# Kernel tuning notes

Measured on AMD Instinct MI355X. Metric: run time of the kernel, lower is better.

Reference implementation:

```python
import jax, jax.numpy as jnp
import numpy as np

NUM_ATOMS = 100
D = 32        # initial_atom_dim
H = 16        # hidden_dim (multiplicity per irrep)
NB = 16       # edge_dim / number of bessel basis functions
CUT = 6.0     # radius_cutoff
DEG = 4.0     # degree_norm
OUT = 1       # output_dim
INV4PI = 1.0 / np.sqrt(4.0 * np.pi)  # 'integral' SH normalization


def _bessel(d, nb, cut):
    # e3nn soft_one_hot_linspace(basis='bessel', cutoff=True) * sqrt(nb)
    x = d[:, None]
    n = jnp.arange(1, nb + 1, dtype=d.dtype)
    safe = jnp.maximum(x, 1e-9)
    out = np.sqrt(2.0 / cut) * jnp.sin(n * jnp.pi * x / cut) / safe
    return out * (x < cut) * np.sqrt(float(nb))


def _fc(x, w1, w2):
    # e3nn FullyConnectedNet: fan-in normalized linear layers, silu, no bias
    h = jax.nn.silu(x @ w1 / np.sqrt(x.shape[-1]))
    return h @ w2 / np.sqrt(w1.shape[-1])


def _forward(atomic_numbers, edge_index, coords, atom_emb,
             fc0_w1, fc0_w2, fc1_w1, fc1_w2, w_readout):
    src, dst = edge_index[0], edge_index[1]
    N = coords.shape[0]
    E = src.shape[0]

    vec = coords[src] - coords[dst]                      # [E,3]
    dist = jnp.linalg.norm(vec, axis=-1)                 # [E]
    unit = vec / jnp.maximum(dist, 1e-9)[:, None]

    # spherical harmonics, l=0 and l=1, 'integral' normalization
    y0 = jnp.full((E,), INV4PI, dtype=coords.dtype)      # [E]
    y1 = (np.sqrt(3.0) * INV4PI) * unit                  # [E,3]
    basis = _bessel(dist, NB, CUT)                       # [E,NB]

    x = atom_emb[atomic_numbers]                         # [N,D] (row 0 is padding)

    # ---- layer 0: scalars (D x0e) x (1x0e+1x1o) -> H x0e + H x1o ----
    w = _fc(basis, fc0_w1, fc0_w2)                       # [E, 2*D*H] per-edge TP weights
    wa = w[:, : D * H].reshape(E, D, H)
    wb = w[:, D * H:].reshape(E, D, H)
    xs = x[src]
    n0 = 1.0 / np.sqrt(D)                                # path fan-in norm
    m0 = jnp.einsum('ed,edh->eh', xs, wa) * y0[:, None] * n0          # [E,H]
    m1 = jnp.einsum('ed,edh->eh', xs, wb)[:, :, None] * y1[:, None, :] * n0  # [E,H,3]
    z0 = jax.ops.segment_sum(m0, dst, num_segments=N) / DEG           # [N,H]
    z1 = jax.ops.segment_sum(m1, dst, num_segments=N) / DEG           # [N,H,3]

    # ---- layer 1: (H x0e + H x1o) x (1x0e+1x1o) -> same irreps, skip-connected ----
    w = _fc(basis, fc1_w1, fc1_w2)                       # [E, 4*H*H]
    w1_ = w[:, 0 * H * H:1 * H * H].reshape(E, H, H)     # 0e x 0e -> 0e
    w2_ = w[:, 1 * H * H:2 * H * H].reshape(E, H, H)     # 0e x 1o -> 1o
    w3_ = w[:, 2 * H * H:3 * H * H].reshape(E, H, H)     # 1o x 0e -> 1o
    w4_ = w[:, 3 * H * H:4 * H * H].reshape(E, H, H)     # 1o x 1o -> 0e (CG = dot/sqrt(3))
    s, v = z0[src], z1[src]
    n1 = 1.0 / np.sqrt(2 * H)                            # two paths per output irrep
    dot = jnp.einsum('ehm,em->eh', v, y1) / np.sqrt(3.0)
    o0 = (jnp.einsum('eh,ehk->ek', s, w1_) * y0[:, None]
          + jnp.einsum('eh,ehk->ek', dot, w4_)) * n1
    o1 = (jnp.einsum('eh,ehk->ek', s, w2_)[:, :, None] * y1[:, None, :]
          + jnp.einsum('ehm,ehk->ekm', v, w3_) * y0[:, None, None]) * n1
    z0 = jax.ops.segment_sum(o0, dst, num_segments=N) / DEG + z0      # skip
    z1 = jax.ops.segment_sum(o1, dst, num_segments=N) / DEG + z1

    # ---- scalar readout (o3.Linear onto 0e) + graph sum-pool ----
    node_scalar = z0 @ w_readout / np.sqrt(H)            # [N,OUT]
    return jnp.sum(node_scalar, axis=0)                  # [OUT]


def setup_inputs() -> dict:
    key = jax.random.key(0)
    ks = jax.random.split(key, 9)
    N, E = 10000, 160000
    atomic_numbers = jax.random.randint(ks[0], (N,), 0, NUM_ATOMS)
    coords = jax.random.normal(ks[1], (N, 3), dtype=jnp.float32)
    edge_index = jax.random.randint(ks[2], (2, E), 0, N)
    atom_emb = jax.random.normal(ks[3], (NUM_ATOMS, D), dtype=jnp.float32).at[0].set(0.0)
    fc0_w1 = jax.random.normal(ks[4], (NB, H), dtype=jnp.float32)
    fc0_w2 = jax.random.normal(ks[5], (H, 2 * D * H), dtype=jnp.float32)
    fc1_w1 = jax.random.normal(ks[6], (NB, H), dtype=jnp.float32)
    fc1_w2 = jax.random.normal(ks[7], (H, 4 * H * H), dtype=jnp.float32)
    w_readout = jax.random.normal(ks[8], (H, OUT), dtype=jnp.float32)
    return {"atomic_numbers": atomic_numbers, "coords": coords, "edge_index": edge_index,
            "atom_emb": atom_emb, "fc0_w1": fc0_w1, "fc0_w2": fc0_w2,
            "fc1_w1": fc1_w1, "fc1_w2": fc1_w2, "w_readout": w_readout}


def reference(atomic_numbers, coords, edge_index, atom_emb,
              fc0_w1, fc0_w2, fc1_w1, fc1_w2, w_readout):
    return _forward(atomic_numbers, edge_index, coords, atom_emb,
                    fc0_w1, fc0_w2, fc1_w1, fc1_w2, w_readout)
```

## Files before the change

### kernel.cpp

```cpp
#include <hip/hip_runtime.h>
#include <math.h>


namespace {
constexpr int   NATOMS   = 100;
constexpr int   CAP      = 64;
constexpr float PI_F     = 3.14159265358979323846f;
constexpr float INV4PI_F = 0.28209479177387814f;
constexpr float SQRT3_F  = 1.7320508075688772f;
constexpr float CUT_F    = 6.0f;
constexpr float BASIS_C  = 2.3094010767585034f;
constexpr float N0_F     = 0.17677669529663687f;
constexpr float K0_F = INV4PI_F * N0_F * 0.0625f;
constexpr float K1_F = SQRT3_F * INV4PI_F * N0_F * 0.0625f;
}

__device__ __forceinline__ float silu_fast(float x) {
  return x / (1.0f + __expf(-x));
}

__device__ __forceinline__ float block_reduce_sum(float v) {
  #pragma unroll
  for (int o = 32; o > 0; o >>= 1) v += __shfl_down(v, o, 64);
  __shared__ float ls[8];
  int lane = threadIdx.x & 63;
  int w    = threadIdx.x >> 6;
  if (lane == 0) ls[w] = v;
  __syncthreads();
  float s = 0.f;
  if (threadIdx.x == 0) {
    int nw = (blockDim.x + 63) >> 6;
    for (int i = 0; i < nw; ++i) s += ls[i];
  }
  return s;
}

__global__ void precompute_kernel(const float* __restrict__ atom_emb,
                                  const float* __restrict__ fc0_w2,
                                  const float* __restrict__ fc1_w2,
                                  const float* __restrict__ w_readout,
                                  float* __restrict__ T0, float* __restrict__ T1,
                                  float* __restrict__ G1, float* __restrict__ G4) {
  int b = blockIdx.x;
  int t = threadIdx.x;
  int j = t >> 4;
  int h = t & 15;
  if (b < NATOMS) {
    float s0 = 0.f, s1 = 0.f;
    #pragma unroll
    for (int d = 0; d < 32; ++d) {
      float x = atom_emb[b * 32 + d];
      s0 = fmaf(x, fc0_w2[j * 1024 + d * 16 + h], s0);
      s1 = fmaf(x, fc0_w2[j * 1024 + 512 + d * 16 + h], s1);
    }
    T0[b * 256 + t] = s0;
    T1[b * 256 + t] = s1;
  } else {
    float g1 = 0.f, g4 = 0.f;
    #pragma unroll
    for (int k = 0; k < 16; ++k) {
      float r = w_readout[k];
      g1 = fmaf(fc1_w2[j * 1024 + h * 16 + k], r, g1);
      g4 = fmaf(fc1_w2[j * 1024 + 768 + h * 16 + k], r, g4);
    }
    G1[t] = g1;
    G4[t] = g4;
  }
}

__global__ void bucket_kernel(const int* __restrict__ ei,
                              int* __restrict__ cursor,
                              int* __restrict__ elist, int E) {
  int e = blockIdx.x * blockDim.x + threadIdx.x;
  if (e < E) {
    int d = ei[E + e];
    int pos = atomicAdd(&cursor[d], 1);
    if (pos < CAP) elist[d * CAP + pos] = ei[e];
  }
}

__global__ void __launch_bounds__(256, 4)
gather_kernel(const int* __restrict__ elist,
              const int* __restrict__ cursor,
              const float* __restrict__ coords,
              const int* __restrict__ an,
              const float* __restrict__ fc0_w1,
              const float* __restrict__ T0,
              const float* __restrict__ T1,
              const float* __restrict__ G1t,
              const float* __restrict__ G4t,
              const float* __restrict__ w_readout,
              float* __restrict__ zbuf,
              float* __restrict__ out,
              int N) {
  __shared__ float ggs[512];
  ggs[threadIdx.x]       = G1t[threadIdx.x];
  ggs[256 + threadIdx.x] = G4t[threadIdx.x];
  __syncthreads();

  int wave = threadIdx.x >> 6;
  int lane = threadIdx.x & 63;
  int g    = lane >> 4;
  int t    = lane & 15;
  int base = lane & 48;
  int node = blockIdx.x * 4 + wave;
  bool valid = node < N;

  float w0c[16];
  #pragma unroll
  for (int k = 0; k < 16; ++k) w0c[k] = fc0_w1[k * 16 + t];
  float rr = w_readout[t];

  float cnx = 0.f, cny = 0.f, cnz = 0.f;
  int cnt = 0;
  if (valid) {
    cnx = coords[3 * node + 0];
    cny = coords[3 * node + 1];
    cnz = coords[3 * node + 2];
    cnt = min(cursor[node], CAP);
  }

  const float angc = PI_F / CUT_F;
  float acc0 = 0.f, accx = 0.f, accy = 0.f, accz = 0.f;
  for (int i = g; i < cnt; i += 4) {
    int s = elist[node * CAP + i];
    float vx = coords[3 * s + 0] - cnx;
    float vy = coords[3 * s + 1] - cny;
    float vz = coords[3 * s + 2] - cnz;
    float dist = sqrtf(vx * vx + vy * vy + vz * vz);
    float inv  = 1.0f / fmaxf(dist, 1e-9f);
    float ux = vx * inv, uy = vy * inv, uz = vz * inv;
    float bc = (dist < CUT_F) ? (BASIS_C * inv) : 0.0f;

    float ang = angc * dist;
    float sc = __sinf(ang);
    float tw = 2.0f * __cosf(ang);
    float sp = 0.f, acc = 0.f;
    #pragma unroll
    for (int k = 0; k < 16; ++k) {
      acc = fmaf(sc, w0c[k], acc);
      float sn = fmaf(tw, sc, -sp);
      sp = sc; sc = sn;
    }
    float h0t = silu_fast(acc * bc * 0.25f);

    int a = an[s];
    const float* t0 = T0 + a * 256 + t;
    const float* t1 = T1 + a * 256 + t;
    float u0 = 0.f, u1 = 0.f;
    #pragma unroll
    for (int j = 0; j < 16; ++j) {
      float hj = __shfl(h0t, base + j, 64);
      u0 = fmaf(hj, t0[j * 16], u0);
      u1 = fmaf(hj, t1[j * 16], u1);
    }
    acc0 += u0;
    accx = fmaf(u1, ux, accx);
    accy = fmaf(u1, uy, accy);
    accz = fmaf(u1, uz, accz);
  }
  acc0 += __shfl_xor(acc0, 16, 64); acc0 += __shfl_xor(acc0, 32, 64);
  accx += __shfl_xor(accx, 16, 64); accx += __shfl_xor(accx, 32, 64);
  accy += __shfl_xor(accy, 16, 64); accy += __shfl_xor(accy, 32, 64);
  accz += __shfl_xor(accz, 16, 64); accz += __shfl_xor(accz, 32, 64);

  float srcv = (g == 0) ? acc0 * K0_F
                        : ((g == 1) ? accx : (g == 2) ? accy : accz) * K1_F;
  int tofs = (g == 0) ? 0 : 256;
  float o = 0.f;
  #pragma unroll
  for (int h = 0; h < 16; ++h) {
    float vh = __shfl(srcv, base + h, 64);
    o = fmaf(ggs[tofs + t * 16 + h], vh, o);
  }
  if (valid) zbuf[(size_t)node * 64 + lane] = o;

  float p = (valid && g == 0) ? acc0 * K0_F * rr : 0.f;
  float tot = block_reduce_sum(p);
  if (threadIdx.x == 0) atomicAdd(out, tot * 0.25f);
}

__global__ void __launch_bounds__(256, 4)
phase2_kernel(const int* __restrict__ ei,
              const float* __restrict__ coords,
              const float* __restrict__ fc1_w1,
              const float* __restrict__ zbuf,
              float* __restrict__ out,
              int E) {
  int t = threadIdx.x & 15;
  float w1c[16];
  #pragma unroll
  for (int k = 0; k < 16; ++k) w1c[k] = fc1_w1[k * 16 + t];

  int gid = (blockIdx.x * blockDim.x + threadIdx.x) >> 4;
  int ngroups = (gridDim.x * blockDim.x) >> 4;
  const float angc = PI_F / CUT_F;

  float c = 0.f;
  for (int e = gid; e < E; e += ngroups) {
    int s = ei[e];
    int d = ei[E + e];
    float vx = coords[3 * s + 0] - coords[3 * d + 0];
    float vy = coords[3 * s + 1] - coords[3 * d + 1];
    float vz = coords[3 * s + 2] - coords[3 * d + 2];
    float dist = sqrtf(vx * vx + vy * vy + vz * vz);
    float inv  = 1.0f / fmaxf(dist, 1e-9f);
    float ux = vx * inv, uy = vy * inv, uz = vz * inv;
    float bc = (dist < CUT_F) ? (BASIS_C * inv) : 0.0f;

    float ang = angc * dist;
    float sc = __sinf(ang);
    float tw = 2.0f * __cosf(ang);
    float sp = 0.f, acc = 0.f;
    #pragma unroll
    for (int k = 0; k < 16; ++k) {
      acc = fmaf(sc, w1c[k], acc);
      float sn = fmaf(tw, sc, -sp);
      sp = sc; sc = sn;
    }
    float h1t = silu_fast(acc * bc * 0.25f);

    const float* zb = zbuf + (size_t)s * 64;
    float q  = zb[t];
    float px = zb[16 + t];
    float py = zb[32 + t];
    float pz = zb[48 + t];
    c = fmaf(h1t, fmaf(px, ux, fmaf(py, uy, fmaf(pz, uz, q))), c);
  }
  c *= INV4PI_F * N0_F * (1.0f / 64.0f);
  float tot = block_reduce_sum(c);
  if (threadIdx.x == 0) atomicAdd(out, tot);
}

extern "C" void kernel_launch(void* const* d_in, const int* in_sizes, int n_in,
                              void* d_out, int out_size, void* d_ws, size_t ws_size,
                              hipStream_t stream) {
  const int*   an        = (const int*)d_in[0];
  const float* coords    = (const float*)d_in[1];
  const int*   ei        = (const int*)d_in[2];
  const float* atom_emb  = (const float*)d_in[3];
  const float* fc0_w1    = (const float*)d_in[4];
  const float* fc0_w2    = (const float*)d_in[5];
  const float* fc1_w1    = (const float*)d_in[6];
  const float* fc1_w2    = (const float*)d_in[7];
  const float* w_readout = (const float*)d_in[8];

  int N = in_sizes[0];
  int E = in_sizes[2] / 2;

  float* ws   = (float*)d_ws;
  float* zbuf = ws;
  float* T0   = zbuf + (size_t)N * 64;
  float* T1   = T0 + NATOMS * 256;
  float* G1   = T1 + NATOMS * 256;
  float* G4   = G1 + 256;
  int*   cursor = (int*)(G4 + 256);
  int*   elist  = cursor + N;
  float* out = (float*)d_out;

  hipMemsetAsync(cursor, 0, (size_t)N * sizeof(int), stream);
  hipMemsetAsync(out, 0, sizeof(float), stream);

  precompute_kernel<<<NATOMS + 1, 256, 0, stream>>>(
      atom_emb, fc0_w2, fc1_w2, w_readout, T0, T1, G1, G4);

  int blk = 256;
  bucket_kernel<<<(E + blk - 1) / blk, blk, 0, stream>>>(ei, cursor, elist, E);

  gather_kernel<<<(N + 3) / 4, blk, 0, stream>>>(
      elist, cursor, coords, an, fc0_w1, T0, T1, G1, G4, w_readout,
      zbuf, out, N);

  phase2_kernel<<<2048, blk, 0, stream>>>(ei, coords, fc1_w1, zbuf, out, E);
}
```

Before: 165.8 us.

## Transpose T/G/zbuf layouts for vector loads, prefetch neighbors, shrink gather blocks

The precomputed T0/T1 and G1/G4 tables are stored transposed so that each lane reads its 16 weights as four float4 loads instead of strided scalars. zbuf is interleaved per hidden channel so phase2 fetches q,px,py,pz with a single float4 load. The gather loop software-prefetches the next neighbor's coordinates and atom type. Gather blocks shrink to 128 threads and phase2 uses half as many blocks. In exchange the loop holds more live registers, and the smaller blocks do more shared-memory setup and atomics per node.

```diff
diff --git a/kernel.cpp b/kernel.cpp
--- a/kernel.cpp
+++ b/kernel.cpp
@@ -39,12 +39,13 @@
                                   const float* __restrict__ fc0_w2,
                                   const float* __restrict__ fc1_w2,
                                   const float* __restrict__ w_readout,
-                                  float* __restrict__ T0, float* __restrict__ T1,
-                                  float* __restrict__ G1, float* __restrict__ G4) {
+                                  float* __restrict__ T0T, float* __restrict__ T1T,
+                                  float* __restrict__ G1T, float* __restrict__ G4T) {
   int b = blockIdx.x;
   int t = threadIdx.x;
   int j = t >> 4;
   int h = t & 15;
+  int tidx = h * 16 + j;
   if (b < NATOMS) {
     float s0 = 0.f, s1 = 0.f;
     #pragma unroll
@@ -53,8 +54,8 @@
       s0 = fmaf(x, fc0_w2[j * 1024 + d * 16 + h], s0);
       s1 = fmaf(x, fc0_w2[j * 1024 + 512 + d * 16 + h], s1);
     }
-    T0[b * 256 + t] = s0;
-    T1[b * 256 + t] = s1;
+    T0T[b * 256 + tidx] = s0;
+    T1T[b * 256 + tidx] = s1;
   } else {
     float g1 = 0.f, g4 = 0.f;
     #pragma unroll
@@ -63,8 +64,8 @@
       g1 = fmaf(fc1_w2[j * 1024 + h * 16 + k], r, g1);
       g4 = fmaf(fc1_w2[j * 1024 + 768 + h * 16 + k], r, g4);
     }
-    G1[t] = g1;
-    G4[t] = g4;
+    G1T[h * 16 + j] = g1;
+    G4T[h * 16 + j] = g4;
   }
 }
 
@@ -79,23 +80,28 @@
   }
 }
 
-__global__ void __launch_bounds__(256, 4)
+__global__ void __launch_bounds__(128)
 gather_kernel(const int* __restrict__ elist,
               const int* __restrict__ cursor,
               const float* __restrict__ coords,
               const int* __restrict__ an,
               const float* __restrict__ fc0_w1,
-              const float* __restrict__ T0,
-              const float* __restrict__ T1,
-              const float* __restrict__ G1t,
-              const float* __restrict__ G4t,
+              const float* __restrict__ T0T,
+              const float* __restrict__ T1T,
+              const float* __restrict__ G1T,
+              const float* __restrict__ G4T,
               const float* __restrict__ w_readout,
               float* __restrict__ zbuf,
               float* __restrict__ out,
               int N) {
   __shared__ float ggs[512];
-  ggs[threadIdx.x]       = G1t[threadIdx.x];
-  ggs[256 + threadIdx.x] = G4t[threadIdx.x];
+  {
+    int tt = threadIdx.x;
+    ggs[tt]       = G1T[tt];
+    ggs[tt + 128] = G1T[tt + 128];
+    ggs[tt + 256] = G4T[tt];
+    ggs[tt + 384] = G4T[tt + 128];
+  }
   __syncthreads();
 
   int wave = threadIdx.x >> 6;
@@ -103,7 +109,7 @@
   int g    = lane >> 4;
   int t    = lane & 15;
   int base = lane & 48;
-  int node = blockIdx.x * 4 + wave;
+  int node = blockIdx.x * 2 + wave;
   bool valid = node < N;
 
   float w0c[16];
@@ -122,11 +128,24 @@
 
   const float angc = PI_F / CUT_F;
   float acc0 = 0.f, accx = 0.f, accy = 0.f, accz = 0.f;
+
+  int s = (g < cnt) ? elist[node * CAP + g] : 0;
+  float sx = coords[3 * s + 0];
+  float sy = coords[3 * s + 1];
+  float sz = coords[3 * s + 2];
+  int   a  = an[s];
+
   for (int i = g; i < cnt; i += 4) {
-    int s = elist[node * CAP + i];
-    float vx = coords[3 * s + 0] - cnx;
-    float vy = coords[3 * s + 1] - cny;
-    float vz = coords[3 * s + 2] - cnz;
+    int inext = i + 4;
+    int sn = (inext < cnt) ? elist[node * CAP + inext] : 0;
+    float nsx = coords[3 * sn + 0];
+    float nsy = coords[3 * sn + 1];
+    float nsz = coords[3 * sn + 2];
+    int   na  = an[sn];
+
+    float vx = sx - cnx;
+    float vy = sy - cny;
+    float vz = sz - cnz;
     float dist = sqrtf(vx * vx + vy * vy + vz * vz);
     float inv  = 1.0f / fmaxf(dist, 1e-9f);
     float ux = vx * inv, uy = vy * inv, uz = vz * inv;
@@ -139,25 +158,33 @@
     #pragma unroll
     for (int k = 0; k < 16; ++k) {
       acc = fmaf(sc, w0c[k], acc);
-      float sn = fmaf(tw, sc, -sp);
-      sp = sc; sc = sn;
+      float sn2 = fmaf(tw, sc, -sp);
+      sp = sc; sc = sn2;
     }
     float h0t = silu_fast(acc * bc * 0.25f);
 
-    int a = an[s];
-    const float* t0 = T0 + a * 256 + t;
-    const float* t1 = T1 + a * 256 + t;
+    const float4* t0 = (const float4*)(T0T + a * 256 + t * 16);
+    const float4* t1 = (const float4*)(T1T + a * 256 + t * 16);
+    float4 A0 = t0[0], A1 = t0[1], A2 = t0[2], A3 = t0[3];
+    float4 B0 = t1[0], B1 = t1[1], B2 = t1[2], B3 = t1[3];
+    float r0[16] = {A0.x,A0.y,A0.z,A0.w, A1.x,A1.y,A1.z,A1.w,
+                    A2.x,A2.y,A2.z,A2.w, A3.x,A3.y,A3.z,A3.w};
+    float r1[16] = {B0.x,B0.y,B0.z,B0.w, B1.x,B1.y,B1.z,B1.w,
+                    B2.x,B2.y,B2.z,B2.w, B3.x,B3.y,B3.z,B3.w};
+
     float u0 = 0.f, u1 = 0.f;
     #pragma unroll
     for (int j = 0; j < 16; ++j) {
       float hj = __shfl(h0t, base + j, 64);
-      u0 = fmaf(hj, t0[j * 16], u0);
-      u1 = fmaf(hj, t1[j * 16], u1);
+      u0 = fmaf(hj, r0[j], u0);
+      u1 = fmaf(hj, r1[j], u1);
     }
     acc0 += u0;
     accx = fmaf(u1, ux, accx);
     accy = fmaf(u1, uy, accy);
     accz = fmaf(u1, uz, accz);
+
+    s = sn; sx = nsx; sy = nsy; sz = nsz; a = na;
   }
   acc0 += __shfl_xor(acc0, 16, 64); acc0 += __shfl_xor(acc0, 32, 64);
   accx += __shfl_xor(accx, 16, 64); accx += __shfl_xor(accx, 32, 64);
@@ -171,9 +198,9 @@
   #pragma unroll
   for (int h = 0; h < 16; ++h) {
     float vh = __shfl(srcv, base + h, 64);
-    o = fmaf(ggs[tofs + t * 16 + h], vh, o);
-  }
-  if (valid) zbuf[(size_t)node * 64 + lane] = o;
+    o = fmaf(ggs[tofs + h * 16 + t], vh, o);
+  }
+  if (valid) zbuf[(size_t)node * 64 + t * 4 + g] = o;
 
   float p = (valid && g == 0) ? acc0 * K0_F * rr : 0.f;
   float tot = block_reduce_sum(p);
@@ -220,12 +247,8 @@
     }
     float h1t = silu_fast(acc * bc * 0.25f);
 
-    const float* zb = zbuf + (size_t)s * 64;
-    float q  = zb[t];
-    float px = zb[16 + t];
-    float py = zb[32 + t];
-    float pz = zb[48 + t];
-    c = fmaf(h1t, fmaf(px, ux, fmaf(py, uy, fmaf(pz, uz, q))), c);
+    float4 z = ((const float4*)(zbuf + (size_t)s * 64))[t];
+    c = fmaf(h1t, fmaf(z.y, ux, fmaf(z.z, uy, fmaf(z.w, uz, z.x))), c);
   }
   c *= INV4PI_F * N0_F * (1.0f / 64.0f);
   float tot = block_reduce_sum(c);
@@ -250,11 +273,11 @@
 
   float* ws   = (float*)d_ws;
   float* zbuf = ws;
-  float* T0   = zbuf + (size_t)N * 64;
-  float* T1   = T0 + NATOMS * 256;
-  float* G1   = T1 + NATOMS * 256;
-  float* G4   = G1 + 256;
-  int*   cursor = (int*)(G4 + 256);
+  float* T0T  = zbuf + (size_t)N * 64;
+  float* T1T  = T0T + NATOMS * 256;
+  float* G1T  = T1T + NATOMS * 256;
+  float* G4T  = G1T + 256;
+  int*   cursor = (int*)(G4T + 256);
   int*   elist  = cursor + N;
   float* out = (float*)d_out;
 
@@ -262,14 +285,14 @@
   hipMemsetAsync(out, 0, sizeof(float), stream);
 
   precompute_kernel<<<NATOMS + 1, 256, 0, stream>>>(
-      atom_emb, fc0_w2, fc1_w2, w_readout, T0, T1, G1, G4);
+      atom_emb, fc0_w2, fc1_w2, w_readout, T0T, T1T, G1T, G4T);
 
   int blk = 256;
   bucket_kernel<<<(E + blk - 1) / blk, blk, 0, stream>>>(ei, cursor, elist, E);
 
-  gather_kernel<<<(N + 3) / 4, blk, 0, stream>>>(
-      elist, cursor, coords, an, fc0_w1, T0, T1, G1, G4, w_readout,
+  gather_kernel<<<(N + 1) / 2, 128, 0, stream>>>(
+      elist, cursor, coords, an, fc0_w1, T0T, T1T, G1T, G4T, w_readout,
       zbuf, out, N);
 
-  phase2_kernel<<<2048, blk, 0, stream>>>(ei, coords, fc1_w1, zbuf, out, E);
-}
+  phase2_kernel<<<1024, blk, 0, stream>>>(ei, coords, fc1_w1, zbuf, out, E);
+}
```

New measurement: 191.0 us. 1.15x slower.

## Merge setup kernels, process two edges per gather iteration, interleave zbuf for float4 reads

Applied to the files above, without the earlier changes.

Merges the weight-precompute and edge-bucketing kernels into one launch, which removes a launch and its serialization point. The gather loop now handles two edges per iteration so more independent loads and math are in flight. The zbuf layout becomes channel-interleaved, so phase2 reads each source's (q,px,py,pz) with a single float4 load instead of four strided scalar loads. The G matrices are stored transposed to match the new indexing. The costs are higher register pressure in the gather kernel and some wasted work on the padded second edge.

```diff
diff --git a/kernel.cpp b/kernel.cpp
--- a/kernel.cpp
+++ b/kernel.cpp
@@ -35,17 +35,20 @@
   return s;
 }
 
-__global__ void precompute_kernel(const float* __restrict__ atom_emb,
-                                  const float* __restrict__ fc0_w2,
-                                  const float* __restrict__ fc1_w2,
-                                  const float* __restrict__ w_readout,
-                                  float* __restrict__ T0, float* __restrict__ T1,
-                                  float* __restrict__ G1, float* __restrict__ G4) {
+__global__ void setup_kernel(const float* __restrict__ atom_emb,
+                             const float* __restrict__ fc0_w2,
+                             const float* __restrict__ fc1_w2,
+                             const float* __restrict__ w_readout,
+                             const int* __restrict__ ei,
+                             float* __restrict__ T0, float* __restrict__ T1,
+                             float* __restrict__ G1T, float* __restrict__ G4T,
+                             int* __restrict__ cursor, int* __restrict__ elist,
+                             int E) {
   int b = blockIdx.x;
-  int t = threadIdx.x;
-  int j = t >> 4;
-  int h = t & 15;
+  int tt = threadIdx.x;
   if (b < NATOMS) {
+    int j = tt >> 4;
+    int h = tt & 15;
     float s0 = 0.f, s1 = 0.f;
     #pragma unroll
     for (int d = 0; d < 32; ++d) {
@@ -53,9 +56,11 @@
       s0 = fmaf(x, fc0_w2[j * 1024 + d * 16 + h], s0);
       s1 = fmaf(x, fc0_w2[j * 1024 + 512 + d * 16 + h], s1);
     }
-    T0[b * 256 + t] = s0;
-    T1[b * 256 + t] = s1;
-  } else {
+    T0[b * 256 + tt] = s0;
+    T1[b * 256 + tt] = s1;
+  } else if (b == NATOMS) {
+    int j = tt >> 4;
+    int h = tt & 15;
     float g1 = 0.f, g4 = 0.f;
     #pragma unroll
     for (int k = 0; k < 16; ++k) {
@@ -63,19 +68,15 @@
       g1 = fmaf(fc1_w2[j * 1024 + h * 16 + k], r, g1);
       g4 = fmaf(fc1_w2[j * 1024 + 768 + h * 16 + k], r, g4);
     }
-    G1[t] = g1;
-    G4[t] = g4;
-  }
-}
-
-__global__ void bucket_kernel(const int* __restrict__ ei,
-                              int* __restrict__ cursor,
-                              int* __restrict__ elist, int E) {
-  int e = blockIdx.x * blockDim.x + threadIdx.x;
-  if (e < E) {
-    int d = ei[E + e];
-    int pos = atomicAdd(&cursor[d], 1);
-    if (pos < CAP) elist[d * CAP + pos] = ei[e];
+    G1T[h * 16 + j] = g1;
+    G4T[h * 16 + j] = g4;
+  } else {
+    int e = (b - NATOMS - 1) * blockDim.x + tt;
+    if (e < E) {
+      int d = ei[E + e];
+      int pos = atomicAdd(&cursor[d], 1);
+      if (pos < CAP) elist[d * CAP + pos] = ei[e];
+    }
   }
 }
 
@@ -87,15 +88,15 @@
               const float* __restrict__ fc0_w1,
               const float* __restrict__ T0,
               const float* __restrict__ T1,
-              const float* __restrict__ G1t,
-              const float* __restrict__ G4t,
+              const float* __restrict__ G1T,
+              const float* __restrict__ G4T,
               const float* __restrict__ w_readout,
               float* __restrict__ zbuf,
               float* __restrict__ out,
               int N) {
   __shared__ float ggs[512];
-  ggs[threadIdx.x]       = G1t[threadIdx.x];
-  ggs[256 + threadIdx.x] = G4t[threadIdx.x];
+  ggs[threadIdx.x]       = G1T[threadIdx.x];
+  ggs[256 + threadIdx.x] = G4T[threadIdx.x];
   __syncthreads();
 
   int wave = threadIdx.x >> 6;
@@ -119,46 +120,66 @@
     cnz = coords[3 * node + 2];
     cnt = min(cursor[node], CAP);
   }
+  const int* eb = elist + (size_t)(valid ? node : 0) * CAP;
 
   const float angc = PI_F / CUT_F;
   float acc0 = 0.f, accx = 0.f, accy = 0.f, accz = 0.f;
-  for (int i = g; i < cnt; i += 4) {
-    int s = elist[node * CAP + i];
-    float vx = coords[3 * s + 0] - cnx;
-    float vy = coords[3 * s + 1] - cny;
-    float vz = coords[3 * s + 2] - cnz;
-    float dist = sqrtf(vx * vx + vy * vy + vz * vz);
-    float inv  = 1.0f / fmaxf(dist, 1e-9f);
-    float ux = vx * inv, uy = vy * inv, uz = vz * inv;
-    float bc = (dist < CUT_F) ? (BASIS_C * inv) : 0.0f;
-
-    float ang = angc * dist;
-    float sc = __sinf(ang);
-    float tw = 2.0f * __cosf(ang);
-    float sp = 0.f, acc = 0.f;
+
+  for (int i = g; i < cnt; i += 8) {
+    int iB = i + 4;
+    bool hasB = iB < cnt;
+    int sA = eb[i];
+    int sB = hasB ? eb[iB] : sA;
+
+    float pxA = coords[3 * sA + 0], pyA = coords[3 * sA + 1], pzA = coords[3 * sA + 2];
+    float pxB = coords[3 * sB + 0], pyB = coords[3 * sB + 1], pzB = coords[3 * sB + 2];
+    int aA = an[sA], aB = an[sB];
+
+    float vxA = pxA - cnx, vyA = pyA - cny, vzA = pzA - cnz;
+    float vxB = pxB - cnx, vyB = pyB - cny, vzB = pzB - cnz;
+    float dA = sqrtf(vxA * vxA + vyA * vyA + vzA * vzA);
+    float dB = sqrtf(vxB * vxB + vyB * vyB + vzB * vzB);
+    float ivA = 1.0f / fmaxf(dA, 1e-9f);
+    float ivB = 1.0f / fmaxf(dB, 1e-9f);
+    float uxA = vxA * ivA, uyA = vyA * ivA, uzA = vzA * ivA;
+    float uxB = vxB * ivB, uyB = vyB * ivB, uzB = vzB * ivB;
+    float bcA = (dA < CUT_F) ? (BASIS_C * ivA) : 0.0f;
+    float bcB = (dB < CUT_F) ? (BASIS_C * ivB) : 0.0f;
+
+    float angA = angc * dA, angB = angc * dB;
+    float scA = __sinf(angA), twA = 2.0f * __cosf(angA), spA = 0.f, hA = 0.f;
+    float scB = __sinf(angB), twB = 2.0f * __cosf(angB), spB = 0.f, hB = 0.f;
     #pragma unroll
     for (int k = 0; k < 16; ++k) {
-      acc = fmaf(sc, w0c[k], acc);
-      float sn = fmaf(tw, sc, -sp);
-      sp = sc; sc = sn;
-    }
-    float h0t = silu_fast(acc * bc * 0.25f);
-
-    int a = an[s];
-    const float* t0 = T0 + a * 256 + t;
-    const float* t1 = T1 + a * 256 + t;
-    float u0 = 0.f, u1 = 0.f;
+      hA = fmaf(scA, w0c[k], hA);
+      hB = fmaf(scB, w0c[k], hB);
+      float snA = fmaf(twA, scA, -spA); spA = scA; scA = snA;
+      float snB = fmaf(twB, scB, -spB); spB = scB; scB = snB;
+    }
+    float h0A = silu_fast(hA * bcA * 0.25f);
+    float h0B = silu_fast(hB * bcB * 0.25f);
+
+    const float* t0A = T0 + aA * 256 + t;
+    const float* t1A = T1 + aA * 256 + t;
+    const float* t0B = T0 + aB * 256 + t;
+    const float* t1B = T1 + aB * 256 + t;
+    float u0A = 0.f, u1A = 0.f, u0B = 0.f, u1B = 0.f;
     #pragma unroll
     for (int j = 0; j < 16; ++j) {
-      float hj = __shfl(h0t, base + j, 64);
-      u0 = fmaf(hj, t0[j * 16], u0);
-      u1 = fmaf(hj, t1[j * 16], u1);
-    }
-    acc0 += u0;
-    accx = fmaf(u1, ux, accx);
-    accy = fmaf(u1, uy, accy);
-    accz = fmaf(u1, uz, accz);
-  }
+      float hjA = __shfl(h0A, base + j, 64);
+      float hjB = __shfl(h0B, base + j, 64);
+      u0A = fmaf(hjA, t0A[j * 16], u0A);
+      u1A = fmaf(hjA, t1A[j * 16], u1A);
+      u0B = fmaf(hjB, t0B[j * 16], u0B);
+      u1B = fmaf(hjB, t1B[j * 16], u1B);
+    }
+    float mB = hasB ? 1.0f : 0.0f;
+    acc0 += u0A + mB * u0B;
+    accx = fmaf(u1A, uxA, fmaf(mB * u1B, uxB, accx));
+    accy = fmaf(u1A, uyA, fmaf(mB * u1B, uyB, accy));
+    accz = fmaf(u1A, uzA, fmaf(mB * u1B, uzB, accz));
+  }
+
   acc0 += __shfl_xor(acc0, 16, 64); acc0 += __shfl_xor(acc0, 32, 64);
   accx += __shfl_xor(accx, 16, 64); accx += __shfl_xor(accx, 32, 64);
   accy += __shfl_xor(accy, 16, 64); accy += __shfl_xor(accy, 32, 64);
@@ -171,9 +192,9 @@
   #pragma unroll
   for (int h = 0; h < 16; ++h) {
     float vh = __shfl(srcv, base + h, 64);
-    o = fmaf(ggs[tofs + t * 16 + h], vh, o);
-  }
-  if (valid) zbuf[(size_t)node * 64 + lane] = o;
+    o = fmaf(ggs[tofs + h * 16 + t], vh, o);
+  }
+  if (valid) zbuf[(size_t)node * 64 + t * 4 + g] = o;
 
   float p = (valid && g == 0) ? acc0 * K0_F * rr : 0.f;
   float tot = block_reduce_sum(p);
@@ -220,12 +241,8 @@
     }
     float h1t = silu_fast(acc * bc * 0.25f);
 
-    const float* zb = zbuf + (size_t)s * 64;
-    float q  = zb[t];
-    float px = zb[16 + t];
-    float py = zb[32 + t];
-    float pz = zb[48 + t];
-    c = fmaf(h1t, fmaf(px, ux, fmaf(py, uy, fmaf(pz, uz, q))), c);
+    float4 z = ((const float4*)(zbuf + (size_t)s * 64))[t];
+    c = fmaf(h1t, fmaf(z.y, ux, fmaf(z.z, uy, fmaf(z.w, uz, z.x))), c);
   }
   c *= INV4PI_F * N0_F * (1.0f / 64.0f);
   float tot = block_reduce_sum(c);
@@ -252,23 +269,23 @@
   float* zbuf = ws;
   float* T0   = zbuf + (size_t)N * 64;
   float* T1   = T0 + NATOMS * 256;
-  float* G1   = T1 + NATOMS * 256;
-  float* G4   = G1 + 256;
-  int*   cursor = (int*)(G4 + 256);
+  float* G1T  = T1 + NATOMS * 256;
+  float* G4T  = G1T + 256;
+  int*   cursor = (int*)(G4T + 256);
   int*   elist  = cursor + N;
   float* out = (float*)d_out;
 
   hipMemsetAsync(cursor, 0, (size_t)N * sizeof(int), stream);
   hipMemsetAsync(out, 0, sizeof(float), stream);
 
-  precompute_kernel<<<NATOMS + 1, 256, 0, stream>>>(
-      atom_emb, fc0_w2, fc1_w2, w_readout, T0, T1, G1, G4);
-
   int blk = 256;
-  bucket_kernel<<<(E + blk - 1) / blk, blk, 0, stream>>>(ei, cursor, elist, E);
+  int ebkts = (E + blk - 1) / blk;
+  setup_kernel<<<NATOMS + 1 + ebkts, blk, 0, stream>>>(
+      atom_emb, fc0_w2, fc1_w2, w_readout, ei,
+      T0, T1, G1T, G4T, cursor, elist, E);
 
   gather_kernel<<<(N + 3) / 4, blk, 0, stream>>>(
-      elist, cursor, coords, an, fc0_w1, T0, T1, G1, G4, w_readout,
+      elist, cursor, coords, an, fc0_w1, T0, T1, G1T, G4T, w_readout,
       zbuf, out, N);
 
   phase2_kernel<<<2048, blk, 0, stream>>>(ei, coords, fc1_w1, zbuf, out, E);
```

Result: no change. 165.0 us (-0.5%).

## Fuse precompute and bucketing, cache per-edge geometry, interleave zbuf layout

Applied to the files above, without the earlier changes.

Merges the weight precompute and edge bucketing into one setup kernel. That kernel also computes each edge's unit vector and distance once, storing them both in edge order and in the per-destination bucket along with the source atom type. The gather and phase2 kernels then read these records instead of recomputing geometry from coords, which removes scattered coordinate and atom-number gathers and one kernel launch. zbuf is stored interleaved so phase2 loads one float4 per lane. The cost is extra workspace traffic to write and read the edge records.

```diff
diff --git a/kernel.cpp b/kernel.cpp
--- a/kernel.cpp
+++ b/kernel.cpp
@@ -35,17 +35,25 @@
   return s;
 }
 
-__global__ void precompute_kernel(const float* __restrict__ atom_emb,
-                                  const float* __restrict__ fc0_w2,
-                                  const float* __restrict__ fc1_w2,
-                                  const float* __restrict__ w_readout,
-                                  float* __restrict__ T0, float* __restrict__ T1,
-                                  float* __restrict__ G1, float* __restrict__ G4) {
+__global__ void setup_kernel(const float* __restrict__ atom_emb,
+                             const float* __restrict__ fc0_w2,
+                             const float* __restrict__ fc1_w2,
+                             const float* __restrict__ w_readout,
+                             const int* __restrict__ ei,
+                             const float* __restrict__ coords,
+                             const int* __restrict__ an,
+                             float* __restrict__ T0, float* __restrict__ T1,
+                             float* __restrict__ G1T, float* __restrict__ G4T,
+                             int* __restrict__ cursor,
+                             float4* __restrict__ evec,
+                             float4* __restrict__ ebuf,
+                             int* __restrict__ ea,
+                             int E) {
   int b = blockIdx.x;
-  int t = threadIdx.x;
-  int j = t >> 4;
-  int h = t & 15;
+  int tt = threadIdx.x;
   if (b < NATOMS) {
+    int j = tt >> 4;
+    int h = tt & 15;
     float s0 = 0.f, s1 = 0.f;
     #pragma unroll
     for (int d = 0; d < 32; ++d) {
@@ -53,9 +61,11 @@
       s0 = fmaf(x, fc0_w2[j * 1024 + d * 16 + h], s0);
       s1 = fmaf(x, fc0_w2[j * 1024 + 512 + d * 16 + h], s1);
     }
-    T0[b * 256 + t] = s0;
-    T1[b * 256 + t] = s1;
-  } else {
+    T0[b * 256 + tt] = s0;
+    T1[b * 256 + tt] = s1;
+  } else if (b == NATOMS) {
+    int j = tt >> 4;
+    int h = tt & 15;
     float g1 = 0.f, g4 = 0.f;
     #pragma unroll
     for (int k = 0; k < 16; ++k) {
@@ -63,39 +73,45 @@
       g1 = fmaf(fc1_w2[j * 1024 + h * 16 + k], r, g1);
       g4 = fmaf(fc1_w2[j * 1024 + 768 + h * 16 + k], r, g4);
     }
-    G1[t] = g1;
-    G4[t] = g4;
-  }
-}
-
-__global__ void bucket_kernel(const int* __restrict__ ei,
-                              int* __restrict__ cursor,
-                              int* __restrict__ elist, int E) {
-  int e = blockIdx.x * blockDim.x + threadIdx.x;
-  if (e < E) {
-    int d = ei[E + e];
-    int pos = atomicAdd(&cursor[d], 1);
-    if (pos < CAP) elist[d * CAP + pos] = ei[e];
+    G1T[h * 16 + j] = g1;
+    G4T[h * 16 + j] = g4;
+  } else {
+    int e = (b - NATOMS - 1) * blockDim.x + tt;
+    if (e < E) {
+      int s = ei[e];
+      int d = ei[E + e];
+      float vx = coords[3 * s + 0] - coords[3 * d + 0];
+      float vy = coords[3 * s + 1] - coords[3 * d + 1];
+      float vz = coords[3 * s + 2] - coords[3 * d + 2];
+      float dist = sqrtf(vx * vx + vy * vy + vz * vz);
+      float inv  = 1.0f / fmaxf(dist, 1e-9f);
+      float4 rec = make_float4(vx * inv, vy * inv, vz * inv, dist);
+      evec[e] = rec;
+      int pos = atomicAdd(&cursor[d], 1);
+      if (pos < CAP) {
+        ebuf[d * CAP + pos] = rec;
+        ea[d * CAP + pos]   = an[s];
+      }
+    }
   }
 }
 
 __global__ void __launch_bounds__(256, 4)
-gather_kernel(const int* __restrict__ elist,
+gather_kernel(const float4* __restrict__ ebuf,
+              const int* __restrict__ ea,
               const int* __restrict__ cursor,
-              const float* __restrict__ coords,
-              const int* __restrict__ an,
               const float* __restrict__ fc0_w1,
               const float* __restrict__ T0,
               const float* __restrict__ T1,
-              const float* __restrict__ G1t,
-              const float* __restrict__ G4t,
+              const float* __restrict__ G1T,
+              const float* __restrict__ G4T,
               const float* __restrict__ w_readout,
               float* __restrict__ zbuf,
               float* __restrict__ out,
               int N) {
   __shared__ float ggs[512];
-  ggs[threadIdx.x]       = G1t[threadIdx.x];
-  ggs[256 + threadIdx.x] = G4t[threadIdx.x];
+  ggs[threadIdx.x]       = G1T[threadIdx.x];
+  ggs[256 + threadIdx.x] = G4T[threadIdx.x];
   __syncthreads();
 
   int wave = threadIdx.x >> 6;
@@ -111,26 +127,17 @@
   for (int k = 0; k < 16; ++k) w0c[k] = fc0_w1[k * 16 + t];
   float rr = w_readout[t];
 
-  float cnx = 0.f, cny = 0.f, cnz = 0.f;
-  int cnt = 0;
-  if (valid) {
-    cnx = coords[3 * node + 0];
-    cny = coords[3 * node + 1];
-    cnz = coords[3 * node + 2];
-    cnt = min(cursor[node], CAP);
-  }
+  int cnt = valid ? min(cursor[node], CAP) : 0;
+  int nb  = (valid ? node : 0) * CAP;
 
   const float angc = PI_F / CUT_F;
   float acc0 = 0.f, accx = 0.f, accy = 0.f, accz = 0.f;
+
   for (int i = g; i < cnt; i += 4) {
-    int s = elist[node * CAP + i];
-    float vx = coords[3 * s + 0] - cnx;
-    float vy = coords[3 * s + 1] - cny;
-    float vz = coords[3 * s + 2] - cnz;
-    float dist = sqrtf(vx * vx + vy * vy + vz * vz);
-    float inv  = 1.0f / fmaxf(dist, 1e-9f);
-    float ux = vx * inv, uy = vy * inv, uz = vz * inv;
-    float bc = (dist < CUT_F) ? (BASIS_C * inv) : 0.0f;
+    float4 ev = ebuf[nb + i];
+    int    a  = ea[nb + i];
+    float dist = ev.w;
+    float bc = (dist < CUT_F) ? (BASIS_C / fmaxf(dist, 1e-9f)) : 0.0f;
 
     float ang = angc * dist;
     float sc = __sinf(ang);
@@ -144,7 +151,6 @@
     }
     float h0t = silu_fast(acc * bc * 0.25f);
 
-    int a = an[s];
     const float* t0 = T0 + a * 256 + t;
     const float* t1 = T1 + a * 256 + t;
     float u0 = 0.f, u1 = 0.f;
@@ -155,10 +161,11 @@
       u1 = fmaf(hj, t1[j * 16], u1);
     }
     acc0 += u0;
-    accx = fmaf(u1, ux, accx);
-    accy = fmaf(u1, uy, accy);
-    accz = fmaf(u1, uz, accz);
-  }
+    accx = fmaf(u1, ev.x, accx);
+    accy = fmaf(u1, ev.y, accy);
+    accz = fmaf(u1, ev.z, accz);
+  }
+
   acc0 += __shfl_xor(acc0, 16, 64); acc0 += __shfl_xor(acc0, 32, 64);
   accx += __shfl_xor(accx, 16, 64); accx += __shfl_xor(accx, 32, 64);
   accy += __shfl_xor(accy, 16, 64); accy += __shfl_xor(accy, 32, 64);
@@ -171,9 +178,9 @@
   #pragma unroll
   for (int h = 0; h < 16; ++h) {
     float vh = __shfl(srcv, base + h, 64);
-    o = fmaf(ggs[tofs + t * 16 + h], vh, o);
-  }
-  if (valid) zbuf[(size_t)node * 64 + lane] = o;
+    o = fmaf(ggs[tofs + h * 16 + t], vh, o);
+  }
+  if (valid) zbuf[(size_t)node * 64 + t * 4 + g] = o;
 
   float p = (valid && g == 0) ? acc0 * K0_F * rr : 0.f;
   float tot = block_reduce_sum(p);
@@ -182,7 +189,7 @@
 
 __global__ void __launch_bounds__(256, 4)
 phase2_kernel(const int* __restrict__ ei,
-              const float* __restrict__ coords,
+              const float4* __restrict__ evec,
               const float* __restrict__ fc1_w1,
               const float* __restrict__ zbuf,
               float* __restrict__ out,
@@ -199,14 +206,9 @@
   float c = 0.f;
   for (int e = gid; e < E; e += ngroups) {
     int s = ei[e];
-    int d = ei[E + e];
-    float vx = coords[3 * s + 0] - coords[3 * d + 0];
-    float vy = coords[3 * s + 1] - coords[3 * d + 1];
-    float vz = coords[3 * s + 2] - coords[3 * d + 2];
-    float dist = sqrtf(vx * vx + vy * vy + vz * vz);
-    float inv  = 1.0f / fmaxf(dist, 1e-9f);
-    float ux = vx * inv, uy = vy * inv, uz = vz * inv;
-    float bc = (dist < CUT_F) ? (BASIS_C * inv) : 0.0f;
+    float4 ev = evec[e];
+    float dist = ev.w;
+    float bc = (dist < CUT_F) ? (BASIS_C / fmaxf(dist, 1e-9f)) : 0.0f;
 
     float ang = angc * dist;
     float sc = __sinf(ang);
@@ -220,12 +222,8 @@
     }
     float h1t = silu_fast(acc * bc * 0.25f);
 
-    const float* zb = zbuf + (size_t)s * 64;
-    float q  = zb[t];
-    float px = zb[16 + t];
-    float py = zb[32 + t];
-    float pz = zb[48 + t];
-    c = fmaf(h1t, fmaf(px, ux, fmaf(py, uy, fmaf(pz, uz, q))), c);
+    float4 z = ((const float4*)(zbuf + (size_t)s * 64))[t];
+    c = fmaf(h1t, fmaf(z.y, ev.x, fmaf(z.z, ev.y, fmaf(z.w, ev.z, z.x))), c);
   }
   c *= INV4PI_F * N0_F * (1.0f / 64.0f);
   float tot = block_reduce_sum(c);
@@ -248,28 +246,29 @@
   int N = in_sizes[0];
   int E = in_sizes[2] / 2;
 
-  float* ws   = (float*)d_ws;
-  float* zbuf = ws;
-  float* T0   = zbuf + (size_t)N * 64;
-  float* T1   = T0 + NATOMS * 256;
-  float* G1   = T1 + NATOMS * 256;
-  float* G4   = G1 + 256;
-  int*   cursor = (int*)(G4 + 256);
-  int*   elist  = cursor + N;
-  float* out = (float*)d_out;
+  float*  ws   = (float*)d_ws;
+  float*  zbuf = ws;
+  float4* evec = (float4*)(zbuf + (size_t)N * 64);
+  float4* ebuf = evec + E;
+  float*  T0   = (float*)(ebuf + (size_t)N * CAP);
+  float*  T1   = T0 + NATOMS * 256;
+  float*  G1T  = T1 + NATOMS * 256;
+  float*  G4T  = G1T + 256;
+  int*    cursor = (int*)(G4T + 256);
+  int*    ea     = cursor + N;
+  float*  out = (float*)d_out;
 
   hipMemsetAsync(cursor, 0, (size_t)N * sizeof(int), stream);
   hipMemsetAsync(out, 0, sizeof(float), stream);
 
-  precompute_kernel<<<NATOMS + 1, 256, 0, stream>>>(
-      atom_emb, fc0_w2, fc1_w2, w_readout, T0, T1, G1, G4);
-
   int blk = 256;
-  bucket_kernel<<<(E + blk - 1) / blk, blk, 0, stream>>>(ei, cursor, elist, E);
+  int ebkts = (E + blk - 1) / blk;
+  setup_kernel<<<NATOMS + 1 + ebkts, blk, 0, stream>>>(
+      atom_emb, fc0_w2, fc1_w2, w_readout, ei, coords, an,
+      T0, T1, G1T, G4T, cursor, evec, ebuf, ea, E);
 
   gather_kernel<<<(N + 3) / 4, blk, 0, stream>>>(
-      elist, cursor, coords, an, fc0_w1, T0, T1, G1, G4, w_readout,
-      zbuf, out, N);
-
-  phase2_kernel<<<2048, blk, 0, stream>>>(ei, coords, fc1_w1, zbuf, out, E);
-}
+      ebuf, ea, cursor, fc0_w1, T0, T1, G1T, G4T, w_readout, zbuf, out, N);
+
+  phase2_kernel<<<2048, blk, 0, stream>>>(ei, evec, fc1_w1, zbuf, out, E);
+}
```

New measurement: 161.5 us. 1.03x faster.
